# Kernel optimization log

Hardware: AMD Instinct MI355X
Metric: run time of the kernel (lower is better)

Reference implementation:

```python
import jax, jax.numpy as jnp
import numpy as np
import math

B = 524288
D = 4
CTX = 64
HID = 128
IN_DIM = 2 + CTX  # keep_idx len is 2 for every mask
# default_masks_D(4, 10) dedups to exactly these 4 masks (torch module therefore has 4 layers)
KEEP = ((0, 1), (1, 2), (2, 3), (0, 3))
TRANS = ((2, 3), (0, 3), (0, 1), (1, 2))
L = 4


def _mlp(x, W1, b1, W2, b2, W3, b3):
    # MLP(in_dim, out_dim, hidden=128, depth=2): Lin+GELU, Lin+GELU, Lin
    x = jax.nn.gelu(x @ W1 + b1, approximate=False)
    x = jax.nn.gelu(x @ W2 + b2, approximate=False)
    return x @ W3 + b3


def setup_inputs() -> dict:
    key = jax.random.key(0)
    ks = jax.random.split(key, 16)
    theta = jax.random.normal(ks[0], (B, D), dtype=jnp.float32)
    h = jax.random.normal(ks[1], (B, CTX), dtype=jnp.float32)
    p = lambda k, shape: jax.random.normal(k, shape, dtype=jnp.float32) * 0.02
    inp = {"theta": theta, "h": h}
    # stacked per-layer weights for s_net and t_net
    for pref, off in (("s", 2), ("t", 8)):
        inp[pref + "W1"] = p(ks[off + 0], (L, IN_DIM, HID))
        inp[pref + "b1"] = p(ks[off + 1], (L, HID))
        inp[pref + "W2"] = p(ks[off + 2], (L, HID, HID))
        inp[pref + "b2"] = p(ks[off + 3], (L, HID))
        inp[pref + "W3"] = p(ks[off + 4], (L, HID, 2))
        inp[pref + "b3"] = p(ks[off + 5], (L, 2))
    return inp


def reference(theta, h, sW1, sb1, sW2, sb2, sW3, sb3, tW1, tb1, tW2, tb2, tW3, tb3):
    # ConditionalRealNVP.log_prob(theta, h)
    x = theta
    logdet = jnp.zeros(theta.shape[0], dtype=theta.dtype)
    for i in range(L):
        keep = np.array(KEEP[i])
        trans = np.array(TRANS[i])
        xp = jnp.concatenate([x[:, keep], h], axis=1)  # [B, 66]
        s = _mlp(xp, sW1[i], sb1[i], sW2[i], sb2[i], sW3[i], sb3[i])  # [B, 2]
        t = _mlp(xp, tW1[i], tb1[i], tW2[i], tb2[i], tW3[i], tb3[i])  # [B, 2]
        x = x.at[:, trans].set(x[:, trans] * jnp.exp(s) + t)
        logdet = logdet + s.sum(axis=1)
    log_pz = -0.5 * (x ** 2).sum(axis=1) - 0.5 * D * math.log(2 * math.pi)
    return log_pz + logdet
```

## Files before the change

kernel.cpp:

```cpp
#include <hip/hip_runtime.h>
#include <hip/hip_bf16.h>

typedef short short8 __attribute__((ext_vector_type(8)));
typedef float f32x4 __attribute__((ext_vector_type(4)));
typedef float f32x2 __attribute__((ext_vector_type(2)));
typedef unsigned short u16;
typedef unsigned int u32;
typedef u32 u32x4 __attribute__((ext_vector_type(4)));

#define NL_STRIDE 57344
#define OFF_W1F 0
#define OFF_W2F 16384
#define OFF_W3F 49152
#define OFF_W1K 53248
#define OFF_B1  54272
#define OFF_B2  54784
#define OFF_B3  55296

__device__ __forceinline__ u16 f2bf(float f) {
  union { float f; unsigned int u; } v; v.f = f;
  unsigned int r = v.u + 0x7fffu + ((v.u >> 16) & 1u);
  return (u16)(r >> 16);
}

__device__ __forceinline__ u32 pack_bf16_2(float a, float b) {
  union { float f; u32 u; } x, y; x.f = a; y.f = b;
  u32 ra = x.u + 0x8000u, rb = y.u + 0x8000u;
  return (ra >> 16) | (rb & 0xffff0000u);
}

__device__ __forceinline__ f32x2 gelu2(f32x2 x) {
  f32x2 u = x * x;
  f32x2 t = u * 0.00417617f + (-0.0560330f);
  t = t * u + 0.394326f;
  f32x2 s = x * t + 0.5f;
  s.x = __builtin_amdgcn_fmed3f(s.x, 0.0f, 1.0f);
  s.y = __builtin_amdgcn_fmed3f(s.y, 0.0f, 1.0f);
  return x * s;
}

__device__ __forceinline__ int kperm(int k) {
  int b = k & 31;
  return (k & ~31) | ((b >> 1) | ((b & 1) << 4));
}

__global__ __launch_bounds__(256) void prep_kernel(
    const float* __restrict__ sW1, const float* __restrict__ sb1,
    const float* __restrict__ sW2, const float* __restrict__ sb2,
    const float* __restrict__ sW3, const float* __restrict__ sb3,
    const float* __restrict__ tW1, const float* __restrict__ tb1,
    const float* __restrict__ tW2, const float* __restrict__ tb2,
    const float* __restrict__ tW3, const float* __restrict__ tb3,
    char* __restrict__ ws)
{
  int nl = blockIdx.x;
  int layer = nl >> 1, net = nl & 1;
  const float* W1 = net ? tW1 : sW1;
  const float* W2 = net ? tW2 : sW2;
  const float* W3 = net ? tW3 : sW3;
  const float* B1 = net ? tb1 : sb1;
  const float* B2 = net ? tb2 : sb2;
  const float* B3 = net ? tb3 : sb3;
  char* base = ws + (size_t)nl * NL_STRIDE;
  int e = blockIdx.y * 256 + (int)threadIdx.x;

  if (e < 8192) {
    int kt = e >> 12, rem = e & 4095, nt = rem >> 9, r2 = rem & 511;
    int l = r2 >> 3, j = r2 & 7;
    int k = kt * 32 + (l >> 4) * 8 + j, n = nt * 16 + (l & 15);
    ((u16*)(base + OFF_W1F))[e] = f2bf(W1[layer * 8448 + (2 + k) * 128 + n]);
  } else if (e < 24576) {
    int e2 = e - 8192;
    int kt = e2 >> 12, nt = (e2 >> 9) & 7, l = (e2 >> 3) & 63, j = e2 & 7;
    int k = kt * 32 + (l >> 4) * 8 + j, n = nt * 16 + (l & 15);
    ((u16*)(base + OFF_W2F))[e2] = f2bf(W2[layer * 16384 + kperm(k) * 128 + n]);
  } else if (e < 26624) {
    int e3 = e - 24576;
    int kt = e3 >> 9, l = (e3 >> 3) & 63, j = e3 & 7;
    int k = kt * 32 + (l >> 4) * 8 + j, n = l & 15;
    float v = (n < 2) ? W3[layer * 256 + kperm(k) * 2 + n] : 0.0f;
    ((u16*)(base + OFF_W3F))[e3] = f2bf(v);
  } else if (e < 26880) {
    int e4 = e - 26624; int r = e4 >> 7, n = e4 & 127;
    ((float*)(base + OFF_W1K))[e4] = W1[layer * 8448 + r * 128 + kperm(n)];
  } else if (e < 27008) {
    int e5 = e - 26880; ((float*)(base + OFF_B1))[e5] = B1[layer * 128 + kperm(e5)];
  } else if (e < 27136) {
    int e6 = e - 27008; ((float*)(base + OFF_B2))[e6] = B2[layer * 128 + kperm(e6)];
  } else if (e < 27138) {
    int e7 = e - 27136; ((float*)(base + OFF_B3))[e7] = B3[layer * 2 + e7];
  }
}

__global__ __launch_bounds__(512, 4) void realnvp_kernel(
    const float* __restrict__ theta, const float* __restrict__ h_g,
    const char* __restrict__ ws, float* __restrict__ out)
{
  __shared__ __align__(16) u16 hs[128 * 72];
  __shared__ __align__(16) u16 hid[128 * 136];
  __shared__ __align__(16) float x_lds[128 * 4];
  __shared__ float sbuf[2 * 128 * 2];

  const int tid = (int)threadIdx.x;
  const int row0 = (int)blockIdx.x * 128;
  const int wave = tid >> 6, lane = tid & 63, q = lane >> 4, lr = lane & 15;
  const int mh = wave & 1, nq = wave >> 1;

  if (tid < 128) {
    float4 t4 = *(const float4*)(theta + (size_t)(row0 + tid) * 4);
    x_lds[tid * 4 + 0] = t4.x; x_lds[tid * 4 + 1] = t4.y;
    x_lds[tid * 4 + 2] = t4.z; x_lds[tid * 4 + 3] = t4.w;
  }
  {
    int r = tid >> 2, sg = tid & 3;
    const float* src = h_g + (size_t)(row0 + r) * 64 + sg * 16;
    u16* dst = &hs[r * 72 + sg * 16];
#pragma unroll
    for (int c = 0; c < 16; c += 8) {
      float4 f0 = *(const float4*)(src + c);
      float4 f1 = *(const float4*)(src + c + 4);
      u32x4 o;
      o[0] = pack_bf16_2(f0.x, f0.y);
      o[1] = pack_bf16_2(f0.z, f0.w);
      o[2] = pack_bf16_2(f1.x, f1.y);
      o[3] = pack_bf16_2(f1.z, f1.w);
      *(u32x4*)(dst + c) = o;
    }
  }
  __syncthreads();

  float logdet = 0.0f;
  const f32x4 zero4 = {0.f, 0.f, 0.f, 0.f};

#pragma unroll 1
  for (int layer = 0; layer < 4; ++layer) {
    const int k0 = (0x0210 >> (layer * 4)) & 15;
    const int k1 = (0x3321 >> (layer * 4)) & 15;

#pragma unroll 1
    for (int net = 0; net < 2; ++net) {
      const char* base = ws + (size_t)(layer * 2 + net) * NL_STRIDE;
      const u16* w1f = (const u16*)(base + OFF_W1F);
      const u16* w2f = (const u16*)(base + OFF_W2F);
      const u16* w3f = (const u16*)(base + OFF_W3F);
      const float* w1k = (const float*)(base + OFF_W1K);
      const float* b1 = (const float*)(base + OFF_B1);
      const float* b2 = (const float*)(base + OFF_B2);
      const float* b3 = (const float*)(base + OFF_B3);

      f32x4 acc[4][2];
#pragma unroll
      for (int i = 0; i < 4; ++i) { acc[i][0] = zero4; acc[i][1] = zero4; }
      {
        short8 b00 = *(const short8*)(w1f + (0 * 8 + 2 * nq + 0) * 512 + lane * 8);
        short8 b01 = *(const short8*)(w1f + (0 * 8 + 2 * nq + 1) * 512 + lane * 8);
        short8 b10 = *(const short8*)(w1f + (1 * 8 + 2 * nq + 0) * 512 + lane * 8);
        short8 b11 = *(const short8*)(w1f + (1 * 8 + 2 * nq + 1) * 512 + lane * 8);
        const u16* abase = &hs[(64 * mh + lr) * 72 + q * 8];
#pragma unroll
        for (int kt = 0; kt < 2; ++kt) {
          short8 A0 = *(const short8*)(abase + 0 * (16 * 72) + kt * 32);
          short8 A1 = *(const short8*)(abase + 1 * (16 * 72) + kt * 32);
          short8 A2 = *(const short8*)(abase + 2 * (16 * 72) + kt * 32);
          short8 A3 = *(const short8*)(abase + 3 * (16 * 72) + kt * 32);
          short8 b0 = kt ? b10 : b00, b1v = kt ? b11 : b01;
          acc[0][0] = __builtin_amdgcn_mfma_f32_16x16x32_bf16(A0, b0, acc[0][0], 0, 0, 0);
          acc[1][0] = __builtin_amdgcn_mfma_f32_16x16x32_bf16(A1, b0, acc[1][0], 0, 0, 0);
          acc[2][0] = __builtin_amdgcn_mfma_f32_16x16x32_bf16(A2, b0, acc[2][0], 0, 0, 0);
          acc[3][0] = __builtin_amdgcn_mfma_f32_16x16x32_bf16(A3, b0, acc[3][0], 0, 0, 0);
          acc[0][1] = __builtin_amdgcn_mfma_f32_16x16x32_bf16(A0, b1v, acc[0][1], 0, 0, 0);
          acc[1][1] = __builtin_amdgcn_mfma_f32_16x16x32_bf16(A1, b1v, acc[1][1], 0, 0, 0);
          acc[2][1] = __builtin_amdgcn_mfma_f32_16x16x32_bf16(A2, b1v, acc[2][1], 0, 0, 0);
          acc[3][1] = __builtin_amdgcn_mfma_f32_16x16x32_bf16(A3, b1v, acc[3][1], 0, 0, 0);
        }
      }
      f32x2 wk0 = *(const f32x2*)(w1k + nq * 32 + 2 * lr);
      f32x2 wk1 = *(const f32x2*)(w1k + 128 + nq * 32 + 2 * lr);
      f32x2 bb  = *(const f32x2*)(b1 + nq * 32 + 2 * lr);
#pragma unroll
      for (int i = 0; i < 4; ++i)
#pragma unroll
        for (int r = 0; r < 4; ++r) {
          int row = 64 * mh + 16 * i + q * 4 + r;
          float xk0 = x_lds[row * 4 + k0], xk1 = x_lds[row * 4 + k1];
          f32x2 v = {acc[i][0][r], acc[i][1][r]};
          v = wk0 * xk0 + v;
          v = wk1 * xk1 + v;
          v = v + bb;
          f32x2 g = gelu2(v);
          ((u32*)&hid[row * 136])[nq * 16 + lr] = pack_bf16_2(g.x, g.y);
        }
      __syncthreads();

      f32x4 acc2[4][2];
#pragma unroll
      for (int i = 0; i < 4; ++i) { acc2[i][0] = zero4; acc2[i][1] = zero4; }
      {
        const u16* hbase = &hid[(64 * mh + lr) * 136 + q * 8];
        short8 nb0 = *(const short8*)(w2f + (0 * 8 + 2 * nq + 0) * 512 + lane * 8);
        short8 nb1 = *(const short8*)(w2f + (0 * 8 + 2 * nq + 1) * 512 + lane * 8);
        short8 pb0 = *(const short8*)(w2f + (1 * 8 + 2 * nq + 0) * 512 + lane * 8);
        short8 pb1 = *(const short8*)(w2f + (1 * 8 + 2 * nq + 1) * 512 + lane * 8);
#pragma unroll
        for (int kt = 0; kt < 4; ++kt) {
          short8 b0 = nb0, b1v = nb1;
          nb0 = pb0; nb1 = pb1;
          if (kt < 2) {
            pb0 = *(const short8*)(w2f + ((kt + 2) * 8 + 2 * nq + 0) * 512 + lane * 8);
            pb1 = *(const short8*)(w2f + ((kt + 2) * 8 + 2 * nq + 1) * 512 + lane * 8);
          }
          short8 A0 = *(const short8*)(hbase + 0 * (16 * 136) + kt * 32);
          short8 A1 = *(const short8*)(hbase + 1 * (16 * 136) + kt * 32);
          short8 A2 = *(const short8*)(hbase + 2 * (16 * 136) + kt * 32);
          short8 A3 = *(const short8*)(hbase + 3 * (16 * 136) + kt * 32);
          acc2[0][0] = __builtin_amdgcn_mfma_f32_16x16x32_bf16(A0, b0, acc2[0][0], 0, 0, 0);
          acc2[1][0] = __builtin_amdgcn_mfma_f32_16x16x32_bf16(A1, b0, acc2[1][0], 0, 0, 0);
          acc2[2][0] = __builtin_amdgcn_mfma_f32_16x16x32_bf16(A2, b0, acc2[2][0], 0, 0, 0);
          acc2[3][0] = __builtin_amdgcn_mfma_f32_16x16x32_bf16(A3, b0, acc2[3][0], 0, 0, 0);
          acc2[0][1] = __builtin_amdgcn_mfma_f32_16x16x32_bf16(A0, b1v, acc2[0][1], 0, 0, 0);
          acc2[1][1] = __builtin_amdgcn_mfma_f32_16x16x32_bf16(A1, b1v, acc2[1][1], 0, 0, 0);
          acc2[2][1] = __builtin_amdgcn_mfma_f32_16x16x32_bf16(A2, b1v, acc2[2][1], 0, 0, 0);
          acc2[3][1] = __builtin_amdgcn_mfma_f32_16x16x32_bf16(A3, b1v, acc2[3][1], 0, 0, 0);
        }
      }
      f32x2 cb = *(const f32x2*)(b2 + nq * 32 + 2 * lr);
      __syncthreads();
#pragma unroll
      for (int i = 0; i < 4; ++i)
#pragma unroll
        for (int r = 0; r < 4; ++r) {
          int row = 64 * mh + 16 * i + q * 4 + r;
          f32x2 v = {acc2[i][0][r], acc2[i][1][r]};
          f32x2 g = gelu2(v + cb);
          ((u32*)&hid[row * 136])[nq * 16 + lr] = pack_bf16_2(g.x, g.y);
        }
      __syncthreads();

      f32x4 acc3 = zero4;
      {
        const u16* hbase3 = &hid[(16 * wave + lr) * 136 + q * 8];
#pragma unroll
        for (int kt = 0; kt < 4; ++kt) {
          short8 b = *(const short8*)(w3f + kt * 512 + lane * 8);
          short8 a = *(const short8*)(hbase3 + kt * 32);
          acc3 = __builtin_amdgcn_mfma_f32_16x16x32_bf16(a, b, acc3, 0, 0, 0);
        }
      }
      if (lr < 2) {
        float bbs = b3[lr];
        int rb = 16 * wave + q * 4;
#pragma unroll
        for (int r = 0; r < 4; ++r)
          sbuf[net * 256 + (rb + r) * 2 + lr] = acc3[r] + bbs;
      }
      __syncthreads();
    }

    if (tid < 128) {
      float s0 = sbuf[tid * 2 + 0], s1 = sbuf[tid * 2 + 1];
      float t0 = sbuf[256 + tid * 2 + 0], t1 = sbuf[256 + tid * 2 + 1];
      const int a0 = (0x1002 >> (layer * 4)) & 15;
      const int a1 = (0x2133 >> (layer * 4)) & 15;
      x_lds[tid * 4 + a0] = x_lds[tid * 4 + a0] * __expf(s0) + t0;
      x_lds[tid * 4 + a1] = x_lds[tid * 4 + a1] * __expf(s1) + t1;
      logdet += s0 + s1;
    }
    __syncthreads();
  }

  if (tid < 128) {
    float x0 = x_lds[tid * 4 + 0], x1 = x_lds[tid * 4 + 1];
    float x2 = x_lds[tid * 4 + 2], x3 = x_lds[tid * 4 + 3];
    out[row0 + tid] = -0.5f * (x0 * x0 + x1 * x1 + x2 * x2 + x3 * x3)
                      - 3.6757541328f + logdet;
  }
}

extern "C" void kernel_launch(void* const* d_in, const int* in_sizes, int n_in,
                              void* d_out, int out_size, void* d_ws, size_t ws_size,
                              hipStream_t stream) {
  (void)in_sizes; (void)n_in; (void)out_size; (void)ws_size;
  const float* theta = (const float*)d_in[0];
  const float* h     = (const float*)d_in[1];
  const float* sW1 = (const float*)d_in[2],  *sb1 = (const float*)d_in[3];
  const float* sW2 = (const float*)d_in[4],  *sb2 = (const float*)d_in[5];
  const float* sW3 = (const float*)d_in[6],  *sb3 = (const float*)d_in[7];
  const float* tW1 = (const float*)d_in[8],  *tb1 = (const float*)d_in[9];
  const float* tW2 = (const float*)d_in[10], *tb2 = (const float*)d_in[11];
  const float* tW3 = (const float*)d_in[12], *tb3 = (const float*)d_in[13];
  float* out = (float*)d_out;
  char* ws = (char*)d_ws;

  dim3 pgrid(8, 107);
  prep_kernel<<<pgrid, 256, 0, stream>>>(sW1, sb1, sW2, sb2, sW3, sb3,
                                         tW1, tb1, tW2, tb2, tW3, tb3, ws);
  realnvp_kernel<<<4096, 512, 0, stream>>>(theta, h, (const char*)ws, out);
}
```

Measured before the change: 617.7 us.

## Keep h fragments in registers, fold theta into MFMA, swizzle double-buffered hidden LDS

Loads the h context directly into per-wave bf16 MFMA A-fragments in registers, so the LDS staging buffer for h goes away. The two theta columns are folded into an extra MFMA using a packed raw W1 slice (new prep entries), and the biases are preloaded into the accumulators. Hidden activations now use two separate LDS buffers with an XOR-swizzled column layout, which removes one barrier per net and is meant to cut bank conflicts. In exchange it adds register pressure and a few near-empty MFMAs, and the theta term is now rounded to bf16.

```diff
diff --git a/kernel.cpp b/kernel.cpp
--- a/kernel.cpp
+++ b/kernel.cpp
@@ -16,6 +16,7 @@
 #define OFF_B1  54272
 #define OFF_B2  54784
 #define OFF_B3  55296
+#define OFF_W1KRAW 56320
 
 __device__ __forceinline__ u16 f2bf(float f) {
   union { float f; unsigned int u; } v; v.f = f;
@@ -89,6 +90,9 @@
     int e6 = e - 27008; ((float*)(base + OFF_B2))[e6] = B2[layer * 128 + kperm(e6)];
   } else if (e < 27138) {
     int e7 = e - 27136; ((float*)(base + OFF_B3))[e7] = B3[layer * 2 + e7];
+  } else if (e < 27394) {
+    int e8 = e - 27138; int n = e8 >> 1, r = e8 & 1;
+    ((float*)(base + OFF_W1KRAW))[e8] = W1[layer * 8448 + r * 128 + n];
   }
 }
 
@@ -96,8 +100,8 @@
     const float* __restrict__ theta, const float* __restrict__ h_g,
     const char* __restrict__ ws, float* __restrict__ out)
 {
-  __shared__ __align__(16) u16 hs[128 * 72];
-  __shared__ __align__(16) u16 hid[128 * 136];
+  __shared__ __align__(16) u16 hidA[128 * 136];
+  __shared__ __align__(16) u16 hidB[128 * 136];
   __shared__ __align__(16) float x_lds[128 * 4];
   __shared__ float sbuf[2 * 128 * 2];
 
@@ -105,37 +109,46 @@
   const int row0 = (int)blockIdx.x * 128;
   const int wave = tid >> 6, lane = tid & 63, q = lane >> 4, lr = lane & 15;
   const int mh = wave & 1, nq = wave >> 1;
+  u32* const hidAw = (u32*)hidA;
+  u32* const hidBw = (u32*)hidB;
 
   if (tid < 128) {
     float4 t4 = *(const float4*)(theta + (size_t)(row0 + tid) * 4);
     x_lds[tid * 4 + 0] = t4.x; x_lds[tid * 4 + 1] = t4.y;
     x_lds[tid * 4 + 2] = t4.z; x_lds[tid * 4 + 3] = t4.w;
   }
-  {
-    int r = tid >> 2, sg = tid & 3;
-    const float* src = h_g + (size_t)(row0 + r) * 64 + sg * 16;
-    u16* dst = &hs[r * 72 + sg * 16];
-#pragma unroll
-    for (int c = 0; c < 16; c += 8) {
-      float4 f0 = *(const float4*)(src + c);
-      float4 f1 = *(const float4*)(src + c + 4);
-      u32x4 o;
-      o[0] = pack_bf16_2(f0.x, f0.y);
-      o[1] = pack_bf16_2(f0.z, f0.w);
-      o[2] = pack_bf16_2(f1.x, f1.y);
-      o[3] = pack_bf16_2(f1.z, f1.w);
-      *(u32x4*)(dst + c) = o;
-    }
-  }
+
+  short8 hfr[4][2];
+#pragma unroll
+  for (int i = 0; i < 4; ++i)
+#pragma unroll
+    for (int kt = 0; kt < 2; ++kt) {
+      const float* src = h_g + (size_t)(row0 + 64 * mh + 16 * i + lr) * 64 + kt * 32 + q * 8;
+      float4 f0 = *(const float4*)(src);
+      float4 f1 = *(const float4*)(src + 4);
+      union { u32x4 u; short8 s; } cv;
+      cv.u[0] = pack_bf16_2(f0.x, f0.y);
+      cv.u[1] = pack_bf16_2(f0.z, f0.w);
+      cv.u[2] = pack_bf16_2(f1.x, f1.y);
+      cv.u[3] = pack_bf16_2(f1.z, f1.w);
+      hfr[i][kt] = cv.s;
+    }
   __syncthreads();
 
   float logdet = 0.0f;
-  const f32x4 zero4 = {0.f, 0.f, 0.f, 0.f};
 
 #pragma unroll 1
   for (int layer = 0; layer < 4; ++layer) {
     const int k0 = (0x0210 >> (layer * 4)) & 15;
     const int k1 = (0x3321 >> (layer * 4)) & 15;
+
+    u32 a2[4];
+#pragma unroll
+    for (int i = 0; i < 4; ++i) {
+      int row = 64 * mh + 16 * i + lr;
+      float xa = x_lds[row * 4 + k0], xb = x_lds[row * 4 + k1];
+      a2[i] = (q == 0) ? pack_bf16_2(xa, xb) : 0u;
+    }
 
 #pragma unroll 1
     for (int net = 0; net < 2; ++net) {
@@ -143,115 +156,99 @@
       const u16* w1f = (const u16*)(base + OFF_W1F);
       const u16* w2f = (const u16*)(base + OFF_W2F);
       const u16* w3f = (const u16*)(base + OFF_W3F);
-      const float* w1k = (const float*)(base + OFF_W1K);
       const float* b1 = (const float*)(base + OFF_B1);
       const float* b2 = (const float*)(base + OFF_B2);
       const float* b3 = (const float*)(base + OFF_B3);
+      const float* w1kraw = (const float*)(base + OFF_W1KRAW);
 
       f32x4 acc[4][2];
-#pragma unroll
-      for (int i = 0; i < 4; ++i) { acc[i][0] = zero4; acc[i][1] = zero4; }
       {
-        short8 b00 = *(const short8*)(w1f + (0 * 8 + 2 * nq + 0) * 512 + lane * 8);
-        short8 b01 = *(const short8*)(w1f + (0 * 8 + 2 * nq + 1) * 512 + lane * 8);
-        short8 b10 = *(const short8*)(w1f + (1 * 8 + 2 * nq + 0) * 512 + lane * 8);
-        short8 b11 = *(const short8*)(w1f + (1 * 8 + 2 * nq + 1) * 512 + lane * 8);
-        const u16* abase = &hs[(64 * mh + lr) * 72 + q * 8];
+        f32x2 bb = *(const f32x2*)(b1 + nq * 32 + 2 * lr);
+#pragma unroll
+        for (int i = 0; i < 4; ++i) {
+          acc[i][0] = (f32x4){bb.x, bb.x, bb.x, bb.x};
+          acc[i][1] = (f32x4){bb.y, bb.y, bb.y, bb.y};
+        }
+        f32x2 wr0 = *(const f32x2*)(w1kraw + 2 * (nq * 32 + lr));
+        f32x2 wr1 = *(const f32x2*)(w1kraw + 2 * (nq * 32 + 16 + lr));
+        union { u32x4 u; short8 s; } bx0, bx1;
+        bx0.u = (u32x4){(q == 0) ? pack_bf16_2(wr0.x, wr0.y) : 0u, 0u, 0u, 0u};
+        bx1.u = (u32x4){(q == 0) ? pack_bf16_2(wr1.x, wr1.y) : 0u, 0u, 0u, 0u};
 #pragma unroll
         for (int kt = 0; kt < 2; ++kt) {
-          short8 A0 = *(const short8*)(abase + 0 * (16 * 72) + kt * 32);
-          short8 A1 = *(const short8*)(abase + 1 * (16 * 72) + kt * 32);
-          short8 A2 = *(const short8*)(abase + 2 * (16 * 72) + kt * 32);
-          short8 A3 = *(const short8*)(abase + 3 * (16 * 72) + kt * 32);
-          short8 b0 = kt ? b10 : b00, b1v = kt ? b11 : b01;
-          acc[0][0] = __builtin_amdgcn_mfma_f32_16x16x32_bf16(A0, b0, acc[0][0], 0, 0, 0);
-          acc[1][0] = __builtin_amdgcn_mfma_f32_16x16x32_bf16(A1, b0, acc[1][0], 0, 0, 0);
-          acc[2][0] = __builtin_amdgcn_mfma_f32_16x16x32_bf16(A2, b0, acc[2][0], 0, 0, 0);
-          acc[3][0] = __builtin_amdgcn_mfma_f32_16x16x32_bf16(A3, b0, acc[3][0], 0, 0, 0);
-          acc[0][1] = __builtin_amdgcn_mfma_f32_16x16x32_bf16(A0, b1v, acc[0][1], 0, 0, 0);
-          acc[1][1] = __builtin_amdgcn_mfma_f32_16x16x32_bf16(A1, b1v, acc[1][1], 0, 0, 0);
-          acc[2][1] = __builtin_amdgcn_mfma_f32_16x16x32_bf16(A2, b1v, acc[2][1], 0, 0, 0);
-          acc[3][1] = __builtin_amdgcn_mfma_f32_16x16x32_bf16(A3, b1v, acc[3][1], 0, 0, 0);
-        }
-      }
-      f32x2 wk0 = *(const f32x2*)(w1k + nq * 32 + 2 * lr);
-      f32x2 wk1 = *(const f32x2*)(w1k + 128 + nq * 32 + 2 * lr);
-      f32x2 bb  = *(const f32x2*)(b1 + nq * 32 + 2 * lr);
+          short8 b0 = *(const short8*)(w1f + (kt * 8 + 2 * nq + 0) * 512 + lane * 8);
+          short8 b1v = *(const short8*)(w1f + (kt * 8 + 2 * nq + 1) * 512 + lane * 8);
+#pragma unroll
+          for (int i = 0; i < 4; ++i) {
+            acc[i][0] = __builtin_amdgcn_mfma_f32_16x16x32_bf16(hfr[i][kt], b0, acc[i][0], 0, 0, 0);
+            acc[i][1] = __builtin_amdgcn_mfma_f32_16x16x32_bf16(hfr[i][kt], b1v, acc[i][1], 0, 0, 0);
+          }
+        }
+#pragma unroll
+        for (int i = 0; i < 4; ++i) {
+          union { u32x4 u; short8 s; } ax;
+          ax.u = (u32x4){a2[i], 0u, 0u, 0u};
+          acc[i][0] = __builtin_amdgcn_mfma_f32_16x16x32_bf16(ax.s, bx0.s, acc[i][0], 0, 0, 0);
+          acc[i][1] = __builtin_amdgcn_mfma_f32_16x16x32_bf16(ax.s, bx1.s, acc[i][1], 0, 0, 0);
+        }
+      }
 #pragma unroll
       for (int i = 0; i < 4; ++i)
 #pragma unroll
         for (int r = 0; r < 4; ++r) {
-          int row = 64 * mh + 16 * i + q * 4 + r;
-          float xk0 = x_lds[row * 4 + k0], xk1 = x_lds[row * 4 + k1];
+          int row = 64 * mh + 16 * i + 4 * q + r;
           f32x2 v = {acc[i][0][r], acc[i][1][r]};
-          v = wk0 * xk0 + v;
-          v = wk1 * xk1 + v;
-          v = v + bb;
           f32x2 g = gelu2(v);
-          ((u32*)&hid[row * 136])[nq * 16 + lr] = pack_bf16_2(g.x, g.y);
+          hidAw[row * 68 + ((nq ^ r) << 4) + lr] = pack_bf16_2(g.x, g.y);
         }
       __syncthreads();
 
       f32x4 acc2[4][2];
-#pragma unroll
-      for (int i = 0; i < 4; ++i) { acc2[i][0] = zero4; acc2[i][1] = zero4; }
       {
-        const u16* hbase = &hid[(64 * mh + lr) * 136 + q * 8];
-        short8 nb0 = *(const short8*)(w2f + (0 * 8 + 2 * nq + 0) * 512 + lane * 8);
-        short8 nb1 = *(const short8*)(w2f + (0 * 8 + 2 * nq + 1) * 512 + lane * 8);
-        short8 pb0 = *(const short8*)(w2f + (1 * 8 + 2 * nq + 0) * 512 + lane * 8);
-        short8 pb1 = *(const short8*)(w2f + (1 * 8 + 2 * nq + 1) * 512 + lane * 8);
-#pragma unroll
-        for (int kt = 0; kt < 4; ++kt) {
-          short8 b0 = nb0, b1v = nb1;
-          nb0 = pb0; nb1 = pb1;
-          if (kt < 2) {
-            pb0 = *(const short8*)(w2f + ((kt + 2) * 8 + 2 * nq + 0) * 512 + lane * 8);
-            pb1 = *(const short8*)(w2f + ((kt + 2) * 8 + 2 * nq + 1) * 512 + lane * 8);
-          }
-          short8 A0 = *(const short8*)(hbase + 0 * (16 * 136) + kt * 32);
-          short8 A1 = *(const short8*)(hbase + 1 * (16 * 136) + kt * 32);
-          short8 A2 = *(const short8*)(hbase + 2 * (16 * 136) + kt * 32);
-          short8 A3 = *(const short8*)(hbase + 3 * (16 * 136) + kt * 32);
-          acc2[0][0] = __builtin_amdgcn_mfma_f32_16x16x32_bf16(A0, b0, acc2[0][0], 0, 0, 0);
-          acc2[1][0] = __builtin_amdgcn_mfma_f32_16x16x32_bf16(A1, b0, acc2[1][0], 0, 0, 0);
-          acc2[2][0] = __builtin_amdgcn_mfma_f32_16x16x32_bf16(A2, b0, acc2[2][0], 0, 0, 0);
-          acc2[3][0] = __builtin_amdgcn_mfma_f32_16x16x32_bf16(A3, b0, acc2[3][0], 0, 0, 0);
-          acc2[0][1] = __builtin_amdgcn_mfma_f32_16x16x32_bf16(A0, b1v, acc2[0][1], 0, 0, 0);
-          acc2[1][1] = __builtin_amdgcn_mfma_f32_16x16x32_bf16(A1, b1v, acc2[1][1], 0, 0, 0);
-          acc2[2][1] = __builtin_amdgcn_mfma_f32_16x16x32_bf16(A2, b1v, acc2[2][1], 0, 0, 0);
-          acc2[3][1] = __builtin_amdgcn_mfma_f32_16x16x32_bf16(A3, b1v, acc2[3][1], 0, 0, 0);
-        }
-      }
-      f32x2 cb = *(const f32x2*)(b2 + nq * 32 + 2 * lr);
+        f32x2 cb = *(const f32x2*)(b2 + nq * 32 + 2 * lr);
+#pragma unroll
+        for (int i = 0; i < 4; ++i) {
+          acc2[i][0] = (f32x4){cb.x, cb.x, cb.x, cb.x};
+          acc2[i][1] = (f32x4){cb.y, cb.y, cb.y, cb.y};
+        }
+      }
+#pragma unroll
+      for (int kt = 0; kt < 4; ++kt) {
+        short8 b0 = *(const short8*)(w2f + (kt * 8 + 2 * nq + 0) * 512 + lane * 8);
+        short8 b1v = *(const short8*)(w2f + (kt * 8 + 2 * nq + 1) * 512 + lane * 8);
+        const int kx = (kt ^ (lr & 3)) << 4;
+#pragma unroll
+        for (int i = 0; i < 4; ++i) {
+          const short8 Ai = *(const short8*)(hidAw + (64 * mh + 16 * i + lr) * 68 + kx + q * 4);
+          acc2[i][0] = __builtin_amdgcn_mfma_f32_16x16x32_bf16(Ai, b0, acc2[i][0], 0, 0, 0);
+          acc2[i][1] = __builtin_amdgcn_mfma_f32_16x16x32_bf16(Ai, b1v, acc2[i][1], 0, 0, 0);
+        }
+      }
+#pragma unroll
+      for (int i = 0; i < 4; ++i)
+#pragma unroll
+        for (int r = 0; r < 4; ++r) {
+          int row = 64 * mh + 16 * i + 4 * q + r;
+          f32x2 v = {acc2[i][0][r], acc2[i][1][r]};
+          f32x2 g = gelu2(v);
+          hidBw[row * 68 + ((nq ^ r) << 4) + lr] = pack_bf16_2(g.x, g.y);
+        }
       __syncthreads();
-#pragma unroll
-      for (int i = 0; i < 4; ++i)
-#pragma unroll
-        for (int r = 0; r < 4; ++r) {
-          int row = 64 * mh + 16 * i + q * 4 + r;
-          f32x2 v = {acc2[i][0][r], acc2[i][1][r]};
-          f32x2 g = gelu2(v + cb);
-          ((u32*)&hid[row * 136])[nq * 16 + lr] = pack_bf16_2(g.x, g.y);
-        }
-      __syncthreads();
-
-      f32x4 acc3 = zero4;
+
       {
-        const u16* hbase3 = &hid[(16 * wave + lr) * 136 + q * 8];
+        float b3i = b3[lr & 1];
+        f32x4 acc3 = (f32x4){b3i, b3i, b3i, b3i};
 #pragma unroll
         for (int kt = 0; kt < 4; ++kt) {
           short8 b = *(const short8*)(w3f + kt * 512 + lane * 8);
-          short8 a = *(const short8*)(hbase3 + kt * 32);
+          const short8 a = *(const short8*)(hidBw + (16 * wave + lr) * 68 + ((kt ^ (lr & 3)) << 4) + q * 4);
           acc3 = __builtin_amdgcn_mfma_f32_16x16x32_bf16(a, b, acc3, 0, 0, 0);
         }
-      }
-      if (lr < 2) {
-        float bbs = b3[lr];
-        int rb = 16 * wave + q * 4;
-#pragma unroll
-        for (int r = 0; r < 4; ++r)
-          sbuf[net * 256 + (rb + r) * 2 + lr] = acc3[r] + bbs;
+        if (lr < 2) {
+#pragma unroll
+          for (int r = 0; r < 4; ++r)
+            sbuf[net * 256 + (16 * wave + 4 * q + r) * 2 + lr] = acc3[r];
+        }
       }
       __syncthreads();
     }
@@ -291,7 +288,7 @@
   float* out = (float*)d_out;
   char* ws = (char*)d_ws;
 
-  dim3 pgrid(8, 107);
+  dim3 pgrid(8, 108);
   prep_kernel<<<pgrid, 256, 0, stream>>>(sW1, sb1, sW2, sb2, sW3, sb3,
                                          tW1, tb1, tW2, tb2, tW3, tb3, ws);
   realnvp_kernel<<<4096, 512, 0, stream>>>(theta, h, (const char*)ws, out);
```

New measurement: 648.4 us. +5.0%, slower.
